# Performance work log

Measured on AMD Instinct MI355X. Metric: run time of the kernel, lower is better.

## Reference

```python
import jax, jax.numpy as jnp
import numpy as np

A = 200.0          # penalty increment
NUM_STRUCT = 4     # classes 0..3: abutment, girder, deck, parapet
# (i, j, mult): weight[i]+=mult*A and weight[j]+=mult*A when GT says center_z_i < center_z_j
# but prediction says center_z_i >= center_z_j (and both classes present in GT and Pr).
PAIRS = [(0, 1, 1.0), (1, 2, 1.0), (2, 3, 1.0), (0, 2, 2.0), (1, 3, 2.0), (0, 3, 3.0)]


def setup_inputs() -> dict:
    key = jax.random.key(0)
    k1, k2, k3, k4, k5 = jax.random.split(key, 5)
    B, N, C = 16, 65536, 5
    pred = jax.random.normal(k1, (B, N, C), dtype=jnp.float32)
    target = jax.random.randint(k2, (B, N), 0, C, dtype=jnp.int32)
    points = jax.random.normal(k3, (B, N, 9), dtype=jnp.float32)
    pred_previous = jax.random.normal(k4, (B * N, C), dtype=jnp.float32)
    target_previous = jax.random.randint(k5, (B * N,), 0, C, dtype=jnp.int64)
    return {"pred": pred, "target": target, "points": points,
            "pred_previous": pred_previous, "target_previous": target_previous}


def _batch_weights(pred, target, points):
    """Per-batch class weights [B, C] following the original branch logic."""
    B, N, C = pred.shape
    z = points[:, :, 2]                                    # [B, N]
    pred_label = jnp.argmax(pred, axis=-1)                 # [B, N]
    cls = jnp.arange(NUM_STRUCT)
    gt_oh = (target[..., None] == cls).astype(z.dtype)     # [B, N, 4]
    pr_oh = (pred_label[..., None] == cls).astype(z.dtype)
    gt_cnt = gt_oh.sum(axis=1)                             # [B, 4]
    pr_cnt = pr_oh.sum(axis=1)
    gt_mean = jnp.einsum('bn,bnc->bc', z, gt_oh) / jnp.maximum(gt_cnt, 1.0)
    pr_mean = jnp.einsum('bn,bnc->bc', z, pr_oh) / jnp.maximum(pr_cnt, 1.0)
    GT = gt_cnt > 0
    PR = pr_cnt > 0

    w = jnp.ones((B, C), dtype=z.dtype)
    # class predicted but absent in GT
    miss = jnp.logical_and(jnp.logical_not(GT), PR).astype(z.dtype)  # [B, 4]
    w = w.at[:, :NUM_STRUCT].add(A * miss)
    # vertical-order violations
    for i, j, m in PAIRS:
        cond = (GT[:, i] & PR[:, i] & GT[:, j] & PR[:, j]
                & (gt_mean[:, i] < gt_mean[:, j])
                & (pr_mean[:, i] >= pr_mean[:, j]))
        add = (m * A) * cond.astype(z.dtype)
        w = w.at[:, i].add(add).at[:, j].add(add)
    return w


def reference(pred, target, points, pred_previous, target_previous):
    B, N, C = pred.shape
    w = _batch_weights(pred, target, points)               # [B, C]
    # weighted cross-entropy over pred_previous, computed once via per-class sums
    logp = jax.nn.log_softmax(pred_previous, axis=-1)      # [M, C]
    nll = -jnp.take_along_axis(logp, target_previous[:, None], axis=1)[:, 0]  # [M]
    s = jax.ops.segment_sum(nll, target_previous, num_segments=C)             # [C]
    n = jax.ops.segment_sum(jnp.ones_like(nll), target_previous, num_segments=C)
    # torch mean-reduction weighted CE: sum_n w[t_n]*nll_n / sum_n w[t_n]
    loss_b = (w @ s) / (w @ n)                             # [B]
    return loss_b.sum()
```

## Files before the change

kernel.cpp:

```cpp
#include <hip/hip_runtime.h>
#include <math.h>

#define A_W 200.0f
#define B_BATCH 16
#define N_PTS 65536
#define C_CLS 5
#define BN (B_BATCH * N_PTS)

#define STAT_BLOCKS 1024
#define NLL_BLOCKS 1024
#define TPB 256
#define NLL_BASE 16384


__device__ inline float wave_reduce_f(float v) {
#pragma unroll
    for (int off = 32; off > 0; off >>= 1)
        v += __shfl_down(v, off, 64);
    return v;
}

__global__ __launch_bounds__(TPB)
void main_kernel(const float* __restrict__ pred,
                 const int* __restrict__ target,
                 const float* __restrict__ points,
                 const float* __restrict__ prev,
                 const unsigned* __restrict__ tprev_u32,
                 float* __restrict__ ws) {
    __shared__ float sm[16];
    __shared__ int sflag;
    const int bid = blockIdx.x;
    const int tid = threadIdx.x;
    const int lane = tid & 63;
    const int wv = tid >> 6;

    if (tid < 16) sm[tid] = 0.0f;

    if (bid >= STAT_BLOCKS && wv == 0) {
        unsigned w = tprev_u32[2 * lane + 1];
        unsigned long long bal = __ballot(w != 0u);
        if (tid == 0) sflag = (bal != 0ull) ? 1 : 0;
    }
    __syncthreads();

    if (bid < STAT_BLOCKS) {
        const int b = bid >> 6;
        const int chunk = bid & 63;
        const size_t n0 = (size_t)b * N_PTS + (size_t)chunk * 1024 + (size_t)tid * 4;

        const float4* __restrict__ p4 = (const float4*)(pred + n0 * 5);
        float4 q0 = p4[0], q1 = p4[1], q2 = p4[2], q3 = p4[3], q4 = p4[4];
        const int4 tg = *(const int4*)(target + n0);
        const float* __restrict__ pb = points + n0 * 9;
        float zv[4] = {pb[2], pb[11], pb[20], pb[29]};

        float xs[4][5] = {
            {q0.x, q0.y, q0.z, q0.w, q1.x},
            {q1.y, q1.z, q1.w, q2.x, q2.y},
            {q2.z, q2.w, q3.x, q3.y, q3.z},
            {q3.w, q4.x, q4.y, q4.z, q4.w}};
        int tgt[4] = {tg.x, tg.y, tg.z, tg.w};

        float gc0 = 0, gc1 = 0, gc2 = 0, gc3 = 0;
        float pc0 = 0, pc1 = 0, pc2 = 0, pc3 = 0;
        float gz0 = 0, gz1 = 0, gz2 = 0, gz3 = 0;
        float pz0 = 0, pz1 = 0, pz2 = 0, pz3 = 0;

#pragma unroll
        for (int j = 0; j < 4; ++j) {
            float x0 = xs[j][0], x1 = xs[j][1], x2 = xs[j][2],
                  x3 = xs[j][3], x4 = xs[j][4];
            int am = 0;
            float bv = x0;
            if (x1 > bv) { bv = x1; am = 1; }
            if (x2 > bv) { bv = x2; am = 2; }
            if (x3 > bv) { bv = x3; am = 3; }
            if (x4 > bv) { bv = x4; am = 4; }
            float z = zv[j];
            int t = tgt[j];
            if (t == 0) { gc0 += 1.f; gz0 += z; }
            else if (t == 1) { gc1 += 1.f; gz1 += z; }
            else if (t == 2) { gc2 += 1.f; gz2 += z; }
            else if (t == 3) { gc3 += 1.f; gz3 += z; }
            if (am == 0) { pc0 += 1.f; pz0 += z; }
            else if (am == 1) { pc1 += 1.f; pz1 += z; }
            else if (am == 2) { pc2 += 1.f; pz2 += z; }
            else if (am == 3) { pc3 += 1.f; pz3 += z; }
        }

        float vals[16] = {gc0, gc1, gc2, gc3, pc0, pc1, pc2, pc3,
                          gz0, gz1, gz2, gz3, pz0, pz1, pz2, pz3};
#pragma unroll
        for (int k = 0; k < 16; ++k) {
            float r = wave_reduce_f(vals[k]);
            if (lane == 0) atomicAdd(&sm[k], r);
        }
        __syncthreads();
        if (tid < 16) ws[(size_t)bid * 16 + tid] = sm[tid];
    } else {
        const int nb = bid - STAT_BLOCKS;
        const size_t k0 = (size_t)nb * 1024 + (size_t)tid * 4;
        const int is32 = sflag;

        const float4* __restrict__ p4 = (const float4*)(prev + k0 * 5);
        float4 q0 = p4[0], q1 = p4[1], q2 = p4[2], q3 = p4[3], q4 = p4[4];

        int tgt[4];
        if (is32) {
            int4 tt = *(const int4*)((const int*)tprev_u32 + k0);
            tgt[0] = tt.x; tgt[1] = tt.y; tgt[2] = tt.z; tgt[3] = tt.w;
        } else {
            int4 a = *(const int4*)((const int*)tprev_u32 + 2 * k0);
            int4 c = *(const int4*)((const int*)tprev_u32 + 2 * k0 + 4);
            tgt[0] = a.x; tgt[1] = a.z; tgt[2] = c.x; tgt[3] = c.z;
        }

        float xs[4][5] = {
            {q0.x, q0.y, q0.z, q0.w, q1.x},
            {q1.y, q1.z, q1.w, q2.x, q2.y},
            {q2.z, q2.w, q3.x, q3.y, q3.z},
            {q3.w, q4.x, q4.y, q4.z, q4.w}};

        float s0 = 0, s1 = 0, s2 = 0, s3 = 0, s4 = 0;
        float c0 = 0, c1 = 0, c2 = 0, c3 = 0, c4 = 0;

#pragma unroll
        for (int j = 0; j < 4; ++j) {
            float x0 = xs[j][0], x1 = xs[j][1], x2 = xs[j][2],
                  x3 = xs[j][3], x4 = xs[j][4];
            float m = fmaxf(fmaxf(fmaxf(x0, x1), fmaxf(x2, x3)), x4);
            float e = expf(x0 - m) + expf(x1 - m) + expf(x2 - m) +
                      expf(x3 - m) + expf(x4 - m);
            float lse = m + logf(e);
            int t = tgt[j];
            float xt = x0;
            xt = (t == 1) ? x1 : xt;
            xt = (t == 2) ? x2 : xt;
            xt = (t == 3) ? x3 : xt;
            xt = (t == 4) ? x4 : xt;
            float nll = lse - xt;
            if (t == 0) { s0 += nll; c0 += 1.f; }
            else if (t == 1) { s1 += nll; c1 += 1.f; }
            else if (t == 2) { s2 += nll; c2 += 1.f; }
            else if (t == 3) { s3 += nll; c3 += 1.f; }
            else { s4 += nll; c4 += 1.f; }
        }

        float vals[10] = {s0, s1, s2, s3, s4, c0, c1, c2, c3, c4};
#pragma unroll
        for (int k = 0; k < 10; ++k) {
            float r = wave_reduce_f(vals[k]);
            if (lane == 0) atomicAdd(&sm[k], r);
        }
        __syncthreads();
        if (tid < 10) ws[NLL_BASE + (size_t)tid * 1024 + nb] = sm[tid];
    }
}

__global__ __launch_bounds__(1024)
void final_kernel(const float* __restrict__ ws, float* __restrict__ out) {
    __shared__ float stat[256];
    __shared__ float sn[10];
    const int t = threadIdx.x;
    const int lane = t & 63;
    const int wv = t >> 6;

    if (t < 256) {
        const int b = t >> 4, v = t & 15;
        const float* p = ws + (size_t)(b * 64) * 16 + v;
        float s = 0.0f;
#pragma unroll 8
        for (int i = 0; i < 64; ++i) s += p[(size_t)i * 16];
        stat[t] = s;
    }
    if (wv >= 4 && wv < 14) {
        const int v = wv - 4;
        const float* p = ws + NLL_BASE + (size_t)v * 1024;
        float s = 0.0f;
#pragma unroll
        for (int k = 0; k < 16; ++k) s += p[lane + 64 * k];
        s = wave_reduce_f(s);
        if (lane == 0) sn[v] = s;
    }
    __syncthreads();

    float loss = 0.0f;
    if (t < B_BATCH) {
        const float* st = stat + t * 16;
        float gc[4], pc[4], gm[4], pm[4];
        bool GT[4], PR[4];
        float w[5] = {1.f, 1.f, 1.f, 1.f, 1.f};
#pragma unroll
        for (int c = 0; c < 4; ++c) {
            gc[c] = st[c];
            pc[c] = st[4 + c];
            GT[c] = gc[c] > 0.0f;
            PR[c] = pc[c] > 0.0f;
            gm[c] = st[8 + c] / fmaxf(gc[c], 1.0f);
            pm[c] = st[12 + c] / fmaxf(pc[c], 1.0f);
            if (!GT[c] && PR[c]) w[c] += A_W;
        }
#define PAIR(i, j, mlt)                                                        \
        {                                                                      \
            bool cond = GT[i] && PR[i] && GT[j] && PR[j] &&                    \
                        (gm[i] < gm[j]) && (pm[i] >= pm[j]);                   \
            float add = (mlt) * A_W * (cond ? 1.0f : 0.0f);                    \
            w[i] += add;                                                       \
            w[j] += add;                                                       \
        }
        PAIR(0, 1, 1.0f)
        PAIR(1, 2, 1.0f)
        PAIR(2, 3, 1.0f)
        PAIR(0, 2, 2.0f)
        PAIR(1, 3, 2.0f)
        PAIR(0, 3, 3.0f)
#undef PAIR
        float num = 0.0f, den = 0.0f;
#pragma unroll
        for (int c = 0; c < C_CLS; ++c) {
            num += w[c] * sn[c];
            den += w[c] * sn[5 + c];
        }
        loss = num / den;
    }
    if (wv == 0) {
#pragma unroll
        for (int off = 8; off > 0; off >>= 1)
            loss += __shfl_down(loss, off, 64);
        if (t == 0) out[0] = loss;
    }
}

extern "C" void kernel_launch(void* const* d_in, const int* in_sizes, int n_in,
                              void* d_out, int out_size, void* d_ws, size_t ws_size,
                              hipStream_t stream) {
    const float* pred = (const float*)d_in[0];
    const int* target = (const int*)d_in[1];
    const float* points = (const float*)d_in[2];
    const float* prev = (const float*)d_in[3];
    const unsigned* tprev = (const unsigned*)d_in[4];
    float* ws = (float*)d_ws;
    float* out = (float*)d_out;

    hipLaunchKernelGGL(main_kernel, dim3(STAT_BLOCKS + NLL_BLOCKS), dim3(TPB),
                       0, stream, pred, target, points, prev, tprev, ws);
    hipLaunchKernelGGL(final_kernel, dim3(1), dim3(1024), 0, stream, ws, out);
}
```

Before: 116.4 us.

## Process eight points per thread, interleave stat/NLL blocks, use fast exp/log

Each thread now handles eight points instead of four, which halves the block count and the per-block reduction and atomic overhead. Stat and NLL blocks are interleaved by block index parity so both workloads run concurrently across the GPU. The partial-sum workspace is transposed so the final kernel can read it with float4 loads, and the NLL path uses __expf/__logf intrinsics. The costs are higher register pressure per thread and slightly reduced accuracy from the fast math intrinsics.

```diff
diff --git a/kernel.cpp b/kernel.cpp
--- a/kernel.cpp
+++ b/kernel.cpp
@@ -7,10 +7,13 @@
 #define C_CLS 5
 #define BN (B_BATCH * N_PTS)
 
-#define STAT_BLOCKS 1024
-#define NLL_BLOCKS 1024
 #define TPB 256
-#define NLL_BASE 16384
+#define PPT 8
+#define PPB (TPB * PPT)
+#define STAT_BLOCKS (BN / PPB)
+#define NLL_BLOCKS (BN / PPB)
+#define SPB (N_PTS / PPB)
+#define NLL_BASE (16 * STAT_BLOCKS)
 
 
 __device__ inline float wave_reduce_f(float v) {
@@ -32,34 +35,37 @@
     const int bid = blockIdx.x;
     const int tid = threadIdx.x;
     const int lane = tid & 63;
-    const int wv = tid >> 6;
+    const int is_nll = bid & 1;
 
     if (tid < 16) sm[tid] = 0.0f;
 
-    if (bid >= STAT_BLOCKS && wv == 0) {
+    if (is_nll && tid < 64) {
         unsigned w = tprev_u32[2 * lane + 1];
         unsigned long long bal = __ballot(w != 0u);
         if (tid == 0) sflag = (bal != 0ull) ? 1 : 0;
     }
     __syncthreads();
 
-    if (bid < STAT_BLOCKS) {
-        const int b = bid >> 6;
-        const int chunk = bid & 63;
-        const size_t n0 = (size_t)b * N_PTS + (size_t)chunk * 1024 + (size_t)tid * 4;
-
+    if (!is_nll) {
+        const int sb = bid >> 1;
+        const int b = sb / SPB;
+        const int chunk = sb % SPB;
+        const size_t n0 = (size_t)b * N_PTS + (size_t)chunk * PPB + (size_t)tid * PPT;
+
+        float x[5 * PPT];
         const float4* __restrict__ p4 = (const float4*)(pred + n0 * 5);
-        float4 q0 = p4[0], q1 = p4[1], q2 = p4[2], q3 = p4[3], q4 = p4[4];
-        const int4 tg = *(const int4*)(target + n0);
-        const float* __restrict__ pb = points + n0 * 9;
-        float zv[4] = {pb[2], pb[11], pb[20], pb[29]};
-
-        float xs[4][5] = {
-            {q0.x, q0.y, q0.z, q0.w, q1.x},
-            {q1.y, q1.z, q1.w, q2.x, q2.y},
-            {q2.z, q2.w, q3.x, q3.y, q3.z},
-            {q3.w, q4.x, q4.y, q4.z, q4.w}};
-        int tgt[4] = {tg.x, tg.y, tg.z, tg.w};
+#pragma unroll
+        for (int i = 0; i < 10; ++i) *(float4*)&x[4 * i] = p4[i];
+
+        int tg[PPT];
+        const int4* __restrict__ t4 = (const int4*)(target + n0);
+        *(int4*)&tg[0] = t4[0];
+        *(int4*)&tg[4] = t4[1];
+
+        float zv[PPT];
+        const float* __restrict__ pb = points + n0 * 9 + 2;
+#pragma unroll
+        for (int j = 0; j < PPT; ++j) zv[j] = pb[9 * j];
 
         float gc0 = 0, gc1 = 0, gc2 = 0, gc3 = 0;
         float pc0 = 0, pc1 = 0, pc2 = 0, pc3 = 0;
@@ -67,9 +73,9 @@
         float pz0 = 0, pz1 = 0, pz2 = 0, pz3 = 0;
 
 #pragma unroll
-        for (int j = 0; j < 4; ++j) {
-            float x0 = xs[j][0], x1 = xs[j][1], x2 = xs[j][2],
-                  x3 = xs[j][3], x4 = xs[j][4];
+        for (int j = 0; j < PPT; ++j) {
+            float x0 = x[5 * j], x1 = x[5 * j + 1], x2 = x[5 * j + 2],
+                  x3 = x[5 * j + 3], x4 = x[5 * j + 4];
             int am = 0;
             float bv = x0;
             if (x1 > bv) { bv = x1; am = 1; }
@@ -77,7 +83,7 @@
             if (x3 > bv) { bv = x3; am = 3; }
             if (x4 > bv) { bv = x4; am = 4; }
             float z = zv[j];
-            int t = tgt[j];
+            int t = tg[j];
             if (t == 0) { gc0 += 1.f; gz0 += z; }
             else if (t == 1) { gc1 += 1.f; gz1 += z; }
             else if (t == 2) { gc2 += 1.f; gz2 += z; }
@@ -96,43 +102,45 @@
             if (lane == 0) atomicAdd(&sm[k], r);
         }
         __syncthreads();
-        if (tid < 16) ws[(size_t)bid * 16 + tid] = sm[tid];
+        if (tid < 16) ws[(size_t)tid * STAT_BLOCKS + sb] = sm[tid];
     } else {
-        const int nb = bid - STAT_BLOCKS;
-        const size_t k0 = (size_t)nb * 1024 + (size_t)tid * 4;
+        const int nb = bid >> 1;
+        const size_t k0 = (size_t)nb * PPB + (size_t)tid * PPT;
         const int is32 = sflag;
 
+        float x[5 * PPT];
         const float4* __restrict__ p4 = (const float4*)(prev + k0 * 5);
-        float4 q0 = p4[0], q1 = p4[1], q2 = p4[2], q3 = p4[3], q4 = p4[4];
-
-        int tgt[4];
+#pragma unroll
+        for (int i = 0; i < 10; ++i) *(float4*)&x[4 * i] = p4[i];
+
+        int tg[PPT];
         if (is32) {
-            int4 tt = *(const int4*)((const int*)tprev_u32 + k0);
-            tgt[0] = tt.x; tgt[1] = tt.y; tgt[2] = tt.z; tgt[3] = tt.w;
+            const int4* __restrict__ t4 = (const int4*)((const int*)tprev_u32 + k0);
+            *(int4*)&tg[0] = t4[0];
+            *(int4*)&tg[4] = t4[1];
         } else {
-            int4 a = *(const int4*)((const int*)tprev_u32 + 2 * k0);
-            int4 c = *(const int4*)((const int*)tprev_u32 + 2 * k0 + 4);
-            tgt[0] = a.x; tgt[1] = a.z; tgt[2] = c.x; tgt[3] = c.z;
-        }
-
-        float xs[4][5] = {
-            {q0.x, q0.y, q0.z, q0.w, q1.x},
-            {q1.y, q1.z, q1.w, q2.x, q2.y},
-            {q2.z, q2.w, q3.x, q3.y, q3.z},
-            {q3.w, q4.x, q4.y, q4.z, q4.w}};
+            const int4* __restrict__ t4 =
+                (const int4*)((const int*)tprev_u32 + 2 * k0);
+#pragma unroll
+            for (int i = 0; i < 4; ++i) {
+                int4 a = t4[i];
+                tg[2 * i] = a.x;
+                tg[2 * i + 1] = a.z;
+            }
+        }
 
         float s0 = 0, s1 = 0, s2 = 0, s3 = 0, s4 = 0;
         float c0 = 0, c1 = 0, c2 = 0, c3 = 0, c4 = 0;
 
 #pragma unroll
-        for (int j = 0; j < 4; ++j) {
-            float x0 = xs[j][0], x1 = xs[j][1], x2 = xs[j][2],
-                  x3 = xs[j][3], x4 = xs[j][4];
+        for (int j = 0; j < PPT; ++j) {
+            float x0 = x[5 * j], x1 = x[5 * j + 1], x2 = x[5 * j + 2],
+                  x3 = x[5 * j + 3], x4 = x[5 * j + 4];
             float m = fmaxf(fmaxf(fmaxf(x0, x1), fmaxf(x2, x3)), x4);
-            float e = expf(x0 - m) + expf(x1 - m) + expf(x2 - m) +
-                      expf(x3 - m) + expf(x4 - m);
-            float lse = m + logf(e);
-            int t = tgt[j];
+            float e = __expf(x0 - m) + __expf(x1 - m) + __expf(x2 - m) +
+                      __expf(x3 - m) + __expf(x4 - m);
+            float lse = m + __logf(e);
+            int t = tg[j];
             float xt = x0;
             xt = (t == 1) ? x1 : xt;
             xt = (t == 2) ? x2 : xt;
@@ -153,7 +161,7 @@
             if (lane == 0) atomicAdd(&sm[k], r);
         }
         __syncthreads();
-        if (tid < 10) ws[NLL_BASE + (size_t)tid * 1024 + nb] = sm[tid];
+        if (tid < 10) ws[NLL_BASE + (size_t)tid * NLL_BLOCKS + nb] = sm[tid];
     }
 }
 
@@ -167,18 +175,21 @@
 
     if (t < 256) {
         const int b = t >> 4, v = t & 15;
-        const float* p = ws + (size_t)(b * 64) * 16 + v;
+        const float4* p = (const float4*)(ws + (size_t)v * STAT_BLOCKS + b * SPB);
         float s = 0.0f;
-#pragma unroll 8
-        for (int i = 0; i < 64; ++i) s += p[(size_t)i * 16];
+#pragma unroll
+        for (int i = 0; i < SPB / 4; ++i) {
+            float4 q = p[i];
+            s += q.x + q.y + q.z + q.w;
+        }
         stat[t] = s;
     }
     if (wv >= 4 && wv < 14) {
         const int v = wv - 4;
-        const float* p = ws + NLL_BASE + (size_t)v * 1024;
+        const float* p = ws + NLL_BASE + (size_t)v * NLL_BLOCKS;
         float s = 0.0f;
 #pragma unroll
-        for (int k = 0; k < 16; ++k) s += p[lane + 64 * k];
+        for (int k = 0; k < NLL_BLOCKS / 64; ++k) s += p[lane + 64 * k];
         s = wave_reduce_f(s);
         if (lane == 0) sn[v] = s;
     }
```

Result: slower. 123.8 us (+6.3%).
